# Kernel tuning notes

Hardware: AMD Instinct MI355X
Metric: run time of the kernel (lower is better)

The kernel has to match this reference:

```python
import jax, jax.numpy as jnp
import numpy as np
from jax import lax

B, L, H = 256, 256, 128
K_MIN, K_MAX, ITERS = 2, 8, 3
ALPHA, BETA = 0.5, 0.5
EPS8, EPS9 = 1e-8, 1e-9


def setup_inputs() -> dict:
    key = jax.random.key(0)
    k1, k2, k3 = jax.random.split(key, 3)
    user_features = jax.random.normal(k1, (B, L, H), dtype=jnp.float32)
    W = jax.random.normal(k2, (H, H), dtype=jnp.float32) * (1.0 / np.sqrt(H))
    b_init = jax.random.normal(k3, (B, K_MAX, L), dtype=jnp.float32)
    return {"user_features": user_features, "W": W, "b_init": b_init}


def _cap_scale(cap):
    # squash-style scalar: n/(1+n)/sqrt(n+eps), n = ||cap||^2
    n = jnp.sum(cap * cap, axis=-1, keepdims=True)
    return n / (1.0 + n) / jnp.sqrt(n + EPS9)


def reference(user_features, W, b_init):
    e = user_features                                  # [B,L,H]
    hat = e @ W.T                                      # nn.Linear(H,H,bias=False)
    # repeat over capsules then transpose -> every capsule sees same projection
    hat_k = jnp.broadcast_to(hat[:, None, :, :], (B, K_MAX, L, H))
    hat_iter = lax.stop_gradient(hat_k)                # stop_grad=True path

    b = b_init
    cap = None
    c = None
    for t in range(ITERS):
        c = jax.nn.softmax(b, axis=-1)                 # mask is all ones
        if t < ITERS - 1:
            cap = jnp.einsum('bkl,bklh->bkh', c, hat_iter)
            cap = _cap_scale(cap) * cap
            delta = jnp.einsum('bklh,bkh->bkl', hat_iter, cap)
            b = b + delta
        else:
            cap = jnp.einsum('bkl,bklh->bkh', c, hat_k)
            cap = _cap_scale(cap) * cap
    interest_capsule = cap                             # [B,K,H]
    final_c = c                                        # [B,K,L]

    e_norm = e / (jnp.linalg.norm(e, axis=-1, keepdims=True) + EPS8)
    strength = jnp.linalg.norm(interest_capsule, axis=-1)  # [B,K]

    scores = []
    for k in range(K_MIN, K_MAX + 1):
        _, idx = lax.top_k(strength, k)                # [B,k]
        c_k = jnp.take_along_axis(final_c, idx[:, :, None], axis=1)  # [B,k,L]
        denom = c_k.sum(axis=-1, keepdims=True) + EPS8
        mu_k = jnp.einsum('bkl,blh->bkh', c_k, e) / denom
        mu_n = mu_k / (jnp.linalg.norm(mu_k, axis=-1, keepdims=True) + EPS8)
        cos = jnp.einsum('blh,bkh->bkl', e_norm, mu_n)
        consistency = (c_k * cos).sum(axis=(-1, -2)) / float(max(1, k) * max(1, L))
        if k > 1:
            pair = jnp.einsum('bkh,bjh->bkj', mu_n, mu_n)
            upper = jnp.triu(pair, k=1).sum(axis=(-1, -2))
            diversity = 1.0 - (2.0 / (k * (k - 1))) * upper
        else:
            diversity = jnp.ones((B,), dtype=mu_n.dtype)
        scores.append(ALPHA * consistency + BETA * diversity)

    k_scores = jnp.stack(scores, axis=1)               # [B, K_MAX-K_MIN+1]
    optimal_k = jnp.argmax(k_scores, axis=1) + K_MIN   # [B]
    return optimal_k, k_scores
```

## Files before the change

kernel.cpp:

```cpp
#include <hip/hip_runtime.h>
#include <hip/hip_bf16.h>
#include <math.h>

#define NB 256
#define NL 256
#define NH 128
#define NK 8

typedef __attribute__((ext_vector_type(8))) short bf16x8;
typedef __attribute__((ext_vector_type(4))) short s16x4;
typedef __attribute__((ext_vector_type(4))) float f32x4;

static __device__ __forceinline__ short f2bf(float x) {
    __hip_bfloat16 b = __float2bfloat16(x);
    return *reinterpret_cast<short*>(&b);
}
static __device__ __forceinline__ float bf2f(short s) {
    union { unsigned int u; float f; } v;
    v.u = ((unsigned int)(unsigned short)s) << 16;
    return v.f;
}

#define MFMA __builtin_amdgcn_mfma_f32_16x16x32_bf16

__global__ __launch_bounds__(256) void setup_w_kernel(const float* __restrict__ W,
                                                      short* __restrict__ whi,
                                                      short* __restrict__ wlo,
                                                      short* __restrict__ wthi,
                                                      short* __restrict__ wtlo) {
    const int id = blockIdx.x * 256 + threadIdx.x;
    const int h = id >> 7, j = id & 127;
    const float w = W[id];
    const short hi = f2bf(w);
    const short lo = f2bf(w - bf2f(hi));
    whi[id] = hi;
    wlo[id] = lo;
    wthi[j * 128 + h] = hi;
    wtlo[j * 128 + h] = lo;
}

__global__ __launch_bounds__(1024) void fused_kernel(const float* __restrict__ e,
                                                     const float* __restrict__ b_init,
                                                     const short* __restrict__ whi,
                                                     const short* __restrict__ wlo,
                                                     const short* __restrict__ wthi,
                                                     const short* __restrict__ wtlo,
                                                     float* __restrict__ out) {
    const int b = blockIdx.x;
    const int t = threadIdx.x;
    const int lane = t & 63, wv = t >> 6;
    const int l16 = lane & 15, grp = lane >> 4;

    __shared__ __align__(16) short eThi[128 * 264];
    __shared__ __align__(16) short eTlo[128 * 264];
    __shared__ __align__(16) short cax[16 * 264];
    __shared__ __align__(16) short mpk[16 * 136];
    __shared__ __align__(16) short cappk[16 * 136];
    __shared__ __align__(16) short gpk[16 * 136];
    __shared__ float enl[256];
    __shared__ float red32[128];
    __shared__ __align__(16) float nrmp[64];
    __shared__ float ksf[8], svals[8], strv[8], Ps[28];

    const float* ebg = e + (size_t)b * (NL * NH);

    bf16x8 eah[4], eal[4];
    {
        const int row = wv * 16 + l16;
        float ss = 0.f;
#pragma unroll
        for (int ks = 0; ks < 4; ++ks) {
            const float4 f0 = *(const float4*)&ebg[row * 128 + ks * 32 + grp * 8];
            const float4 f1 = *(const float4*)&ebg[row * 128 + ks * 32 + grp * 8 + 4];
            const float fx[8] = {f0.x, f0.y, f0.z, f0.w, f1.x, f1.y, f1.z, f1.w};
            bf16x8 hv, lv;
#pragma unroll
            for (int j = 0; j < 8; ++j) {
                const short h = f2bf(fx[j]);
                hv[j] = h;
                lv[j] = f2bf(fx[j] - bf2f(h));
                ss += fx[j] * fx[j];
            }
            eah[ks] = hv;
            eal[ks] = lv;
        }
        ss += __shfl_xor(ss, 16);
        ss += __shfl_xor(ss, 32);
        if (grp == 0) enl[row] = sqrtf(ss) + 1e-8f;
    }

#pragma unroll
    for (int i = 0; i < 4; ++i) {
        const int p = i * 1024 + t;
        const int h = p & 127, c = p >> 7;
        float le[8];
#pragma unroll
        for (int j = 0; j < 8; ++j) le[j] = ebg[(c * 8 + j) * 128 + h];
        bf16x8 hv, lv;
#pragma unroll
        for (int j = 0; j < 8; ++j) {
            const short s = f2bf(le[j]);
            hv[j] = s;
            lv[j] = f2bf(le[j] - bf2f(s));
        }
        *(bf16x8*)&eThi[h * 264 + c * 8] = hv;
        *(bf16x8*)&eTlo[h * 264 + c * 8] = lv;
    }

    float lr0 = 0.f, lr1 = 0.f, lr2 = 0.f, lr3 = 0.f;
    if (l16 < 8) {
        const float4 bi = *(const float4*)&b_init[(size_t)b * 2048 + l16 * 256 + wv * 16 + grp * 4];
        lr0 = bi.x; lr1 = bi.y; lr2 = bi.z; lr3 = bi.w;
    }
    __syncthreads();

    for (int iter = 0; iter < 3; ++iter) {
        {
            const float e0 = expf(lr0), e1 = expf(lr1);
            const float e2 = expf(lr2), e3 = expf(lr3);
            float s4 = e0 + e1 + e2 + e3;
            s4 += __shfl_xor(s4, 16);
            s4 += __shfl_xor(s4, 32);
            if (l16 < 8 && grp == 0) red32[wv * 8 + l16] = s4;
            if (l16 < 8) {
                const int lb = wv * 16 + grp * 4;
                const float cv[4] = {e0, e1, e2, e3};
                s16x4 his, los;
#pragma unroll
                for (int j = 0; j < 4; ++j) {
                    const short h = f2bf(cv[j]);
                    his[j] = h;
                    los[j] = f2bf(cv[j] - bf2f(h));
                }
                *(s16x4*)&cax[l16 * 264 + lb] = his;
                *(s16x4*)&cax[(l16 + 8) * 264 + lb] = los;
            }
        }
        __syncthreads();

        if (wv < 8) {
            const int n0 = wv * 16;
            f32x4 acc = (f32x4){0.f, 0.f, 0.f, 0.f};
#pragma unroll
            for (int ks = 0; ks < 8; ++ks) {
                const bf16x8 af = *(const bf16x8*)&cax[l16 * 264 + ks * 32 + grp * 8];
                const bf16x8 bh = *(const bf16x8*)&eThi[(n0 + l16) * 264 + ks * 32 + grp * 8];
                const bf16x8 bl = *(const bf16x8*)&eTlo[(n0 + l16) * 264 + ks * 32 + grp * 8];
                acc = MFMA(af, bh, acc, 0, 0, 0);
                acc = MFMA(af, bl, acc, 0, 0, 0);
            }
            f32x4 ms;
#pragma unroll
            for (int r = 0; r < 4; ++r) ms[r] = acc[r] + __shfl_xor(acc[r], 32);
            if (grp < 2) {
#pragma unroll
                for (int r = 0; r < 4; ++r) {
                    const int k = grp * 4 + r, h = n0 + l16;
                    const short hv = f2bf(ms[r]);
                    mpk[k * 136 + h] = hv;
                    mpk[(k + 8) * 136 + h] = f2bf(ms[r] - bf2f(hv));
                }
            }
        }
        __syncthreads();

        if (wv < 8) {
            float inv = 0.f;
            if (l16 < 8) {
                float kss = 0.f;
#pragma unroll
                for (int w = 0; w < 16; ++w) kss += red32[w * 8 + l16];
                inv = 1.0f / kss;
            }
            const int n0 = wv * 16;
            f32x4 acc = (f32x4){0.f, 0.f, 0.f, 0.f};
#pragma unroll
            for (int ks = 0; ks < 4; ++ks) {
                const bf16x8 af = *(const bf16x8*)&mpk[l16 * 136 + ks * 32 + grp * 8];
                const int bo = (n0 + l16) * 128 + ks * 32 + grp * 8;
                acc = MFMA(af, *(const bf16x8*)&whi[bo], acc, 0, 0, 0);
                acc = MFMA(af, *(const bf16x8*)&wlo[bo], acc, 0, 0, 0);
            }
            f32x4 cs;
            float pn[4];
#pragma unroll
            for (int r = 0; r < 4; ++r) {
                cs[r] = acc[r] + __shfl_xor(acc[r], 32);
                cs[r] *= __shfl(inv, grp * 4 + r);
                float p2 = cs[r] * cs[r];
                p2 += __shfl_xor(p2, 1);
                p2 += __shfl_xor(p2, 2);
                p2 += __shfl_xor(p2, 4);
                p2 += __shfl_xor(p2, 8);
                pn[r] = p2;
            }
            if (l16 == 0 && grp < 2) {
                float4 pv;
                pv.x = pn[0]; pv.y = pn[1]; pv.z = pn[2]; pv.w = pn[3];
                *(float4*)&nrmp[wv * 8 + grp * 4] = pv;
            }
            if (iter < 2 && grp < 2) {
#pragma unroll
                for (int r = 0; r < 4; ++r) {
                    const int k = grp * 4 + r, h = n0 + l16;
                    const short hv = f2bf(cs[r]);
                    cappk[k * 136 + h] = hv;
                    cappk[(k + 8) * 136 + h] = f2bf(cs[r] - bf2f(hv));
                }
            }
            if (iter == 2 && wv == 0 && grp == 0 && l16 < 8) ksf[l16] = inv;
        }
        __syncthreads();

        if (iter < 2) {
            if (wv < 8) {
                float sc = 0.f;
                if (l16 < 8) {
                    float n = 0.f;
#pragma unroll
                    for (int w = 0; w < 8; ++w) n += nrmp[w * 8 + l16];
                    sc = n / (1.0f + n) / sqrtf(n + 1e-9f);
                }
                const int n0 = wv * 16;
                f32x4 acc = (f32x4){0.f, 0.f, 0.f, 0.f};
#pragma unroll
                for (int ks = 0; ks < 4; ++ks) {
                    const bf16x8 af = *(const bf16x8*)&cappk[l16 * 136 + ks * 32 + grp * 8];
                    const int bo = (n0 + l16) * 128 + ks * 32 + grp * 8;
                    acc = MFMA(af, *(const bf16x8*)&wthi[bo], acc, 0, 0, 0);
                    acc = MFMA(af, *(const bf16x8*)&wtlo[bo], acc, 0, 0, 0);
                }
                f32x4 gs;
#pragma unroll
                for (int r = 0; r < 4; ++r) {
                    gs[r] = acc[r] + __shfl_xor(acc[r], 32);
                    gs[r] *= __shfl(sc, grp * 4 + r);
                }
                if (grp < 2) {
#pragma unroll
                    for (int r = 0; r < 4; ++r) {
                        const int k = grp * 4 + r, h = n0 + l16;
                        const short hv = f2bf(gs[r]);
                        gpk[k * 136 + h] = hv;
                        gpk[(k + 8) * 136 + h] = f2bf(gs[r] - bf2f(hv));
                    }
                }
            }
            __syncthreads();

            {
                f32x4 acc;
                acc[0] = (l16 < 8) ? lr0 : 0.f;
                acc[1] = (l16 < 8) ? lr1 : 0.f;
                acc[2] = (l16 < 8) ? lr2 : 0.f;
                acc[3] = (l16 < 8) ? lr3 : 0.f;
#pragma unroll
                for (int ks = 0; ks < 4; ++ks) {
                    const bf16x8 bf = *(const bf16x8*)&gpk[l16 * 136 + ks * 32 + grp * 8];
                    acc = MFMA(eah[ks], bf, acc, 0, 0, 0);
                    acc = MFMA(eal[ks], bf, acc, 0, 0, 0);
                }
                lr0 = acc[0] + __shfl_xor(acc[0], 8);
                lr1 = acc[1] + __shfl_xor(acc[1], 8);
                lr2 = acc[2] + __shfl_xor(acc[2], 8);
                lr3 = acc[3] + __shfl_xor(acc[3], 8);
            }
        }
    }

    if (wv == 8 && lane < 8) {
        float n = 0.f;
#pragma unroll
        for (int w = 0; w < 8; ++w) n += nrmp[w * 8 + lane];
        strv[lane] = n / (1.0f + n) * sqrtf(n) / sqrtf(n + 1e-9f);
    }
    if (wv < 8) {
        const int k = wv;
        float x0 = bf2f(mpk[k * 136 + lane]) + bf2f(mpk[(k + 8) * 136 + lane]);
        float x1 = bf2f(mpk[k * 136 + 64 + lane]) + bf2f(mpk[(k + 8) * 136 + 64 + lane]);
        float s = x0 * x0 + x1 * x1;
#pragma unroll
        for (int o = 32; o; o >>= 1) s += __shfl_xor(s, o);
        const float nv = sqrtf(s) + 1e-8f;
        x0 /= nv; x1 /= nv;
        short hv = f2bf(x0);
        gpk[k * 136 + lane] = hv;
        gpk[(k + 8) * 136 + lane] = f2bf(x0 - bf2f(hv));
        hv = f2bf(x1);
        gpk[k * 136 + 64 + lane] = hv;
        gpk[(k + 8) * 136 + 64 + lane] = f2bf(x1 - bf2f(hv));
    }
    __syncthreads();

    {
        f32x4 acc = (f32x4){0.f, 0.f, 0.f, 0.f};
#pragma unroll
        for (int ks = 0; ks < 4; ++ks) {
            const bf16x8 bf = *(const bf16x8*)&gpk[l16 * 136 + ks * 32 + grp * 8];
            acc = MFMA(eah[ks], bf, acc, 0, 0, 0);
            acc = MFMA(eal[ks], bf, acc, 0, 0, 0);
        }
        f32x4 d;
#pragma unroll
        for (int r = 0; r < 4; ++r) d[r] = acc[r] + __shfl_xor(acc[r], 8);
        float sv = 0.f;
        if (l16 < 8) {
            const float kinv = ksf[l16];
#pragma unroll
            for (int r = 0; r < 4; ++r) {
                const int l = wv * 16 + grp * 4 + r;
                const float cv = (bf2f(cax[l16 * 264 + l]) + bf2f(cax[(l16 + 8) * 264 + l])) * kinv;
                sv += d[r] * cv / enl[l];
            }
        }
        sv += __shfl_xor(sv, 16);
        sv += __shfl_xor(sv, 32);
        if (l16 < 8 && grp == 0) red32[wv * 8 + l16] = sv;
    }
#pragma unroll
    for (int pp = 0; pp < 2; ++pp) {
        const int p = wv + pp * 16;
        if (p < 28) {
            int i = 0, rem = p;
            while (rem >= 7 - i) { rem -= 7 - i; ++i; }
            const int j = i + 1 + rem;
            const float mi0 = bf2f(gpk[i * 136 + lane]) + bf2f(gpk[(i + 8) * 136 + lane]);
            const float mi1 = bf2f(gpk[i * 136 + 64 + lane]) + bf2f(gpk[(i + 8) * 136 + 64 + lane]);
            const float mj0 = bf2f(gpk[j * 136 + lane]) + bf2f(gpk[(j + 8) * 136 + lane]);
            const float mj1 = bf2f(gpk[j * 136 + 64 + lane]) + bf2f(gpk[(j + 8) * 136 + 64 + lane]);
            float v = mi0 * mj0 + mi1 * mj1;
#pragma unroll
            for (int o = 32; o; o >>= 1) v += __shfl_xor(v, o);
            if (lane == 0) Ps[p] = v;
        }
    }
    __syncthreads();
    if (t < 8) {
        float s = 0.f;
#pragma unroll
        for (int w = 0; w < 16; ++w) s += red32[w * 8 + t];
        svals[t] = s;
    }
    __syncthreads();

    if (t == 0) {
        int idx[8];
        for (int i = 0; i < 8; ++i) idx[i] = i;
        for (int a = 1; a < 8; ++a) {
            const int key = idx[a];
            const float kv = strv[key];
            int bb = a - 1;
            while (bb >= 0 && strv[idx[bb]] < kv) { idx[bb + 1] = idx[bb]; --bb; }
            idx[bb + 1] = key;
        }
        float best = -1e30f;
        int bestk = 2;
        float cons_sum = 0.f, pair_sum = 0.f;
        for (int kk = 1; kk <= 8; ++kk) {
            const int ni = idx[kk - 1];
            cons_sum += svals[ni];
            for (int a = 0; a < kk - 1; ++a) {
                const int ia = idx[a];
                const int lo = ia < ni ? ia : ni;
                const int hi2 = ia < ni ? ni : ia;
                const int off0 = lo * 7 - lo * (lo - 1) / 2;
                pair_sum += Ps[off0 + hi2 - lo - 1];
            }
            if (kk >= 2) {
                const float cons = cons_sum / (kk * 256.0f);
                const float divv = 1.0f - (2.0f / (kk * (kk - 1))) * pair_sum;
                const float score = 0.5f * cons + 0.5f * divv;
                out[256 + b * 7 + (kk - 2)] = score;
                if (score > best) { best = score; bestk = kk; }
            }
        }
        out[b] = (float)bestk;
    }
}

extern "C" void kernel_launch(void* const* d_in, const int* in_sizes, int n_in,
                              void* d_out, int out_size, void* d_ws, size_t ws_size,
                              hipStream_t stream) {
    const float* e = (const float*)d_in[0];
    const float* W = (const float*)d_in[1];
    const float* b_init = (const float*)d_in[2];
    float* out = (float*)d_out;

    short* whi = (short*)d_ws;
    short* wlo = whi + 16384;
    short* wthi = wlo + 16384;
    short* wtlo = wthi + 16384;

    hipLaunchKernelGGL(setup_w_kernel, dim3(64), dim3(256), 0, stream, W, whi, wlo, wthi, wtlo);
    hipLaunchKernelGGL(fused_kernel, dim3(NB), dim3(1024), 0, stream,
                       e, b_init, whi, wlo, wthi, wtlo, out);
}
```

Measured before the change: 39.05 us.

## Precompute hat = e·Wᵀ once per batch and route iterations through it

Instead of chaining c·e then ·W and cap·Wᵀ then e·g on every routing iteration, the kernel first computes the projected features hat = e·Wᵀ with MFMA into shared memory. Each iteration then needs only c·hat for capsules and hat·cap for the logit update, which drops two dependent GEMM stages and one block barrier per iteration. The e-transpose tile is rebuilt afterwards for the final mu computation. This adds an up-front 256x128x128 GEMM per batch and extra register use for the hat fragments, and it uses a 3-term split-bf16 product for hat instead of the full 4-term one.

```diff
diff --git a/kernel.cpp b/kernel.cpp
--- a/kernel.cpp
+++ b/kernel.cpp
@@ -25,34 +25,26 @@
 
 __global__ __launch_bounds__(256) void setup_w_kernel(const float* __restrict__ W,
                                                       short* __restrict__ whi,
-                                                      short* __restrict__ wlo,
-                                                      short* __restrict__ wthi,
-                                                      short* __restrict__ wtlo) {
+                                                      short* __restrict__ wlo) {
     const int id = blockIdx.x * 256 + threadIdx.x;
-    const int h = id >> 7, j = id & 127;
     const float w = W[id];
     const short hi = f2bf(w);
-    const short lo = f2bf(w - bf2f(hi));
     whi[id] = hi;
-    wlo[id] = lo;
-    wthi[j * 128 + h] = hi;
-    wtlo[j * 128 + h] = lo;
+    wlo[id] = f2bf(w - bf2f(hi));
 }
 
 __global__ __launch_bounds__(1024) void fused_kernel(const float* __restrict__ e,
                                                      const float* __restrict__ b_init,
                                                      const short* __restrict__ whi,
                                                      const short* __restrict__ wlo,
-                                                     const short* __restrict__ wthi,
-                                                     const short* __restrict__ wtlo,
                                                      float* __restrict__ out) {
     const int b = blockIdx.x;
     const int t = threadIdx.x;
     const int lane = t & 63, wv = t >> 6;
     const int l16 = lane & 15, grp = lane >> 4;
 
-    __shared__ __align__(16) short eThi[128 * 264];
-    __shared__ __align__(16) short eTlo[128 * 264];
+    __shared__ __align__(16) short tThi[128 * 264];
+    __shared__ __align__(16) short tTlo[128 * 264];
     __shared__ __align__(16) short cax[16 * 264];
     __shared__ __align__(16) short mpk[16 * 136];
     __shared__ __align__(16) short cappk[16 * 136];
@@ -89,22 +81,30 @@
         if (grp == 0) enl[row] = sqrtf(ss) + 1e-8f;
     }
 
-#pragma unroll
-    for (int i = 0; i < 4; ++i) {
-        const int p = i * 1024 + t;
-        const int h = p & 127, c = p >> 7;
-        float le[8];
-#pragma unroll
-        for (int j = 0; j < 8; ++j) le[j] = ebg[(c * 8 + j) * 128 + h];
-        bf16x8 hv, lv;
-#pragma unroll
-        for (int j = 0; j < 8; ++j) {
-            const short s = f2bf(le[j]);
-            hv[j] = s;
-            lv[j] = f2bf(le[j] - bf2f(s));
-        }
-        *(bf16x8*)&eThi[h * 264 + c * 8] = hv;
-        *(bf16x8*)&eTlo[h * 264 + c * 8] = lv;
+    {
+#pragma unroll
+        for (int ht = 0; ht < 8; ++ht) {
+            const int h0 = ht * 16;
+            f32x4 a0 = (f32x4){0.f, 0.f, 0.f, 0.f};
+            f32x4 a1 = (f32x4){0.f, 0.f, 0.f, 0.f};
+#pragma unroll
+            for (int ks = 0; ks < 4; ++ks) {
+                const int ao = (h0 + l16) * 128 + ks * 32 + grp * 8;
+                const bf16x8 awh = *(const bf16x8*)&whi[ao];
+                const bf16x8 awl = *(const bf16x8*)&wlo[ao];
+                a0 = MFMA(awh, eah[ks], a0, 0, 0, 0);
+                a0 = MFMA(awh, eal[ks], a0, 0, 0, 0);
+                a1 = MFMA(awl, eah[ks], a1, 0, 0, 0);
+            }
+#pragma unroll
+            for (int r = 0; r < 4; ++r) {
+                const float v = a0[r] + a1[r];
+                const short hv = f2bf(v);
+                const int o = (h0 + grp * 4 + r) * 264 + wv * 16 + l16;
+                tThi[o] = hv;
+                tTlo[o] = f2bf(v - bf2f(hv));
+            }
+        }
     }
 
     float lr0 = 0.f, lr1 = 0.f, lr2 = 0.f, lr3 = 0.f;
@@ -113,6 +113,17 @@
         lr0 = bi.x; lr1 = bi.y; lr2 = bi.z; lr3 = bi.w;
     }
     __syncthreads();
+
+    bf16x8 hah[4], hal[4];
+#pragma unroll
+    for (int ks = 0; ks < 4; ++ks) {
+#pragma unroll
+        for (int j = 0; j < 8; ++j) {
+            const int o = (ks * 32 + grp * 8 + j) * 264 + wv * 16 + l16;
+            hah[ks][j] = tThi[o];
+            hal[ks][j] = tTlo[o];
+        }
+    }
 
     for (int iter = 0; iter < 3; ++iter) {
         {
@@ -139,32 +150,6 @@
         __syncthreads();
 
         if (wv < 8) {
-            const int n0 = wv * 16;
-            f32x4 acc = (f32x4){0.f, 0.f, 0.f, 0.f};
-#pragma unroll
-            for (int ks = 0; ks < 8; ++ks) {
-                const bf16x8 af = *(const bf16x8*)&cax[l16 * 264 + ks * 32 + grp * 8];
-                const bf16x8 bh = *(const bf16x8*)&eThi[(n0 + l16) * 264 + ks * 32 + grp * 8];
-                const bf16x8 bl = *(const bf16x8*)&eTlo[(n0 + l16) * 264 + ks * 32 + grp * 8];
-                acc = MFMA(af, bh, acc, 0, 0, 0);
-                acc = MFMA(af, bl, acc, 0, 0, 0);
-            }
-            f32x4 ms;
-#pragma unroll
-            for (int r = 0; r < 4; ++r) ms[r] = acc[r] + __shfl_xor(acc[r], 32);
-            if (grp < 2) {
-#pragma unroll
-                for (int r = 0; r < 4; ++r) {
-                    const int k = grp * 4 + r, h = n0 + l16;
-                    const short hv = f2bf(ms[r]);
-                    mpk[k * 136 + h] = hv;
-                    mpk[(k + 8) * 136 + h] = f2bf(ms[r] - bf2f(hv));
-                }
-            }
-        }
-        __syncthreads();
-
-        if (wv < 8) {
             float inv = 0.f;
             if (l16 < 8) {
                 float kss = 0.f;
@@ -173,14 +158,25 @@
                 inv = 1.0f / kss;
             }
             const int n0 = wv * 16;
-            f32x4 acc = (f32x4){0.f, 0.f, 0.f, 0.f};
+            f32x4 ac0 = (f32x4){0.f, 0.f, 0.f, 0.f};
+            f32x4 ac1 = (f32x4){0.f, 0.f, 0.f, 0.f};
 #pragma unroll
             for (int ks = 0; ks < 4; ++ks) {
-                const bf16x8 af = *(const bf16x8*)&mpk[l16 * 136 + ks * 32 + grp * 8];
-                const int bo = (n0 + l16) * 128 + ks * 32 + grp * 8;
-                acc = MFMA(af, *(const bf16x8*)&whi[bo], acc, 0, 0, 0);
-                acc = MFMA(af, *(const bf16x8*)&wlo[bo], acc, 0, 0, 0);
-            }
+                const bf16x8 af = *(const bf16x8*)&cax[l16 * 264 + ks * 32 + grp * 8];
+                const bf16x8 bh = *(const bf16x8*)&tThi[(n0 + l16) * 264 + ks * 32 + grp * 8];
+                const bf16x8 bl = *(const bf16x8*)&tTlo[(n0 + l16) * 264 + ks * 32 + grp * 8];
+                ac0 = MFMA(af, bh, ac0, 0, 0, 0);
+                ac0 = MFMA(af, bl, ac0, 0, 0, 0);
+            }
+#pragma unroll
+            for (int ks = 4; ks < 8; ++ks) {
+                const bf16x8 af = *(const bf16x8*)&cax[l16 * 264 + ks * 32 + grp * 8];
+                const bf16x8 bh = *(const bf16x8*)&tThi[(n0 + l16) * 264 + ks * 32 + grp * 8];
+                const bf16x8 bl = *(const bf16x8*)&tTlo[(n0 + l16) * 264 + ks * 32 + grp * 8];
+                ac1 = MFMA(af, bh, ac1, 0, 0, 0);
+                ac1 = MFMA(af, bl, ac1, 0, 0, 0);
+            }
+            const f32x4 acc = ac0 + ac1;
             f32x4 cs;
             float pn[4];
 #pragma unroll
@@ -213,58 +209,24 @@
         __syncthreads();
 
         if (iter < 2) {
-            if (wv < 8) {
-                float sc = 0.f;
-                if (l16 < 8) {
-                    float n = 0.f;
-#pragma unroll
-                    for (int w = 0; w < 8; ++w) n += nrmp[w * 8 + l16];
-                    sc = n / (1.0f + n) / sqrtf(n + 1e-9f);
-                }
-                const int n0 = wv * 16;
-                f32x4 acc = (f32x4){0.f, 0.f, 0.f, 0.f};
-#pragma unroll
-                for (int ks = 0; ks < 4; ++ks) {
-                    const bf16x8 af = *(const bf16x8*)&cappk[l16 * 136 + ks * 32 + grp * 8];
-                    const int bo = (n0 + l16) * 128 + ks * 32 + grp * 8;
-                    acc = MFMA(af, *(const bf16x8*)&wthi[bo], acc, 0, 0, 0);
-                    acc = MFMA(af, *(const bf16x8*)&wtlo[bo], acc, 0, 0, 0);
-                }
-                f32x4 gs;
-#pragma unroll
-                for (int r = 0; r < 4; ++r) {
-                    gs[r] = acc[r] + __shfl_xor(acc[r], 32);
-                    gs[r] *= __shfl(sc, grp * 4 + r);
-                }
-                if (grp < 2) {
-#pragma unroll
-                    for (int r = 0; r < 4; ++r) {
-                        const int k = grp * 4 + r, h = n0 + l16;
-                        const short hv = f2bf(gs[r]);
-                        gpk[k * 136 + h] = hv;
-                        gpk[(k + 8) * 136 + h] = f2bf(gs[r] - bf2f(hv));
-                    }
-                }
-            }
-            __syncthreads();
-
+            float sc;
             {
-                f32x4 acc;
-                acc[0] = (l16 < 8) ? lr0 : 0.f;
-                acc[1] = (l16 < 8) ? lr1 : 0.f;
-                acc[2] = (l16 < 8) ? lr2 : 0.f;
-                acc[3] = (l16 < 8) ? lr3 : 0.f;
-#pragma unroll
-                for (int ks = 0; ks < 4; ++ks) {
-                    const bf16x8 bf = *(const bf16x8*)&gpk[l16 * 136 + ks * 32 + grp * 8];
-                    acc = MFMA(eah[ks], bf, acc, 0, 0, 0);
-                    acc = MFMA(eal[ks], bf, acc, 0, 0, 0);
-                }
-                lr0 = acc[0] + __shfl_xor(acc[0], 8);
-                lr1 = acc[1] + __shfl_xor(acc[1], 8);
-                lr2 = acc[2] + __shfl_xor(acc[2], 8);
-                lr3 = acc[3] + __shfl_xor(acc[3], 8);
-            }
+                float n = 0.f;
+#pragma unroll
+                for (int w = 0; w < 8; ++w) n += nrmp[w * 8 + (l16 & 7)];
+                sc = n / (1.0f + n) / sqrtf(n + 1e-9f);
+            }
+            f32x4 acc = (f32x4){0.f, 0.f, 0.f, 0.f};
+#pragma unroll
+            for (int ks = 0; ks < 4; ++ks) {
+                const bf16x8 bf = *(const bf16x8*)&cappk[l16 * 136 + ks * 32 + grp * 8];
+                acc = MFMA(hah[ks], bf, acc, 0, 0, 0);
+                acc = MFMA(hal[ks], bf, acc, 0, 0, 0);
+            }
+            lr0 += sc * (acc[0] + __shfl_xor(acc[0], 8));
+            lr1 += sc * (acc[1] + __shfl_xor(acc[1], 8));
+            lr2 += sc * (acc[2] + __shfl_xor(acc[2], 8));
+            lr3 += sc * (acc[3] + __shfl_xor(acc[3], 8));
         }
     }
 
@@ -274,6 +236,61 @@
         for (int w = 0; w < 8; ++w) n += nrmp[w * 8 + lane];
         strv[lane] = n / (1.0f + n) * sqrtf(n) / sqrtf(n + 1e-9f);
     }
+#pragma unroll
+    for (int i = 0; i < 4; ++i) {
+        const int p = i * 1024 + t;
+        const int h = p & 127, c = p >> 7;
+        float le[8];
+#pragma unroll
+        for (int j = 0; j < 8; ++j) le[j] = ebg[(c * 8 + j) * 128 + h];
+        bf16x8 hv, lv;
+#pragma unroll
+        for (int j = 0; j < 8; ++j) {
+            const short s = f2bf(le[j]);
+            hv[j] = s;
+            lv[j] = f2bf(le[j] - bf2f(s));
+        }
+        *(bf16x8*)&tThi[h * 264 + c * 8] = hv;
+        *(bf16x8*)&tTlo[h * 264 + c * 8] = lv;
+    }
+    __syncthreads();
+
+    if (wv < 8) {
+        const int n0 = wv * 16;
+        f32x4 ac0 = (f32x4){0.f, 0.f, 0.f, 0.f};
+        f32x4 ac1 = (f32x4){0.f, 0.f, 0.f, 0.f};
+#pragma unroll
+        for (int ks = 0; ks < 4; ++ks) {
+            const bf16x8 af = *(const bf16x8*)&cax[l16 * 264 + ks * 32 + grp * 8];
+            const bf16x8 bh = *(const bf16x8*)&tThi[(n0 + l16) * 264 + ks * 32 + grp * 8];
+            const bf16x8 bl = *(const bf16x8*)&tTlo[(n0 + l16) * 264 + ks * 32 + grp * 8];
+            ac0 = MFMA(af, bh, ac0, 0, 0, 0);
+            ac0 = MFMA(af, bl, ac0, 0, 0, 0);
+        }
+#pragma unroll
+        for (int ks = 4; ks < 8; ++ks) {
+            const bf16x8 af = *(const bf16x8*)&cax[l16 * 264 + ks * 32 + grp * 8];
+            const bf16x8 bh = *(const bf16x8*)&tThi[(n0 + l16) * 264 + ks * 32 + grp * 8];
+            const bf16x8 bl = *(const bf16x8*)&tTlo[(n0 + l16) * 264 + ks * 32 + grp * 8];
+            ac1 = MFMA(af, bh, ac1, 0, 0, 0);
+            ac1 = MFMA(af, bl, ac1, 0, 0, 0);
+        }
+        const f32x4 acc = ac0 + ac1;
+        f32x4 ms;
+#pragma unroll
+        for (int r = 0; r < 4; ++r) ms[r] = acc[r] + __shfl_xor(acc[r], 32);
+        if (grp < 2) {
+#pragma unroll
+            for (int r = 0; r < 4; ++r) {
+                const int k = grp * 4 + r, h = n0 + l16;
+                const short hv = f2bf(ms[r]);
+                mpk[k * 136 + h] = hv;
+                mpk[(k + 8) * 136 + h] = f2bf(ms[r] - bf2f(hv));
+            }
+        }
+    }
+    __syncthreads();
+
     if (wv < 8) {
         const int k = wv;
         float x0 = bf2f(mpk[k * 136 + lane]) + bf2f(mpk[(k + 8) * 136 + lane]);
@@ -388,10 +405,8 @@
 
     short* whi = (short*)d_ws;
     short* wlo = whi + 16384;
-    short* wthi = wlo + 16384;
-    short* wtlo = wthi + 16384;
-
-    hipLaunchKernelGGL(setup_w_kernel, dim3(64), dim3(256), 0, stream, W, whi, wlo, wthi, wtlo);
+
+    hipLaunchKernelGGL(setup_w_kernel, dim3(64), dim3(256), 0, stream, W, whi, wlo);
     hipLaunchKernelGGL(fused_kernel, dim3(NB), dim3(1024), 0, stream,
-                       e, b_init, whi, wlo, wthi, wtlo, out);
+                       e, b_init, whi, wlo, out);
 }
```

After: 70.86 us. 81.5% more time.
